# Kernel tuning notes

Hardware: AMD Instinct MI355X
Metric: run time of the kernel (lower is better)

## Reference

```python
import jax, jax.numpy as jnp
import numpy as np

B, S, D, H = 2, 2048, 1024, 16
DK = D // H


def setup_inputs() -> dict:
    key = jax.random.key(0)
    ks = jax.random.split(key, 11)
    scale = 1.0 / np.sqrt(D)
    inp = {
        "k": jax.random.normal(ks[0], (B, S, D), jnp.float32),
        "q": jax.random.normal(ks[1], (B, S, D), jnp.float32),
        "v": jax.random.normal(ks[2], (B, S, D), jnp.float32),
        "w_q": jax.random.normal(ks[3], (D, D), jnp.float32) * scale,
        "b_q": jax.random.normal(ks[4], (D,), jnp.float32) * 0.01,
        "w_k": jax.random.normal(ks[5], (D, D), jnp.float32) * scale,
        "b_k": jax.random.normal(ks[6], (D,), jnp.float32) * 0.01,
        "w_v": jax.random.normal(ks[7], (D, D), jnp.float32) * scale,
        "b_v": jax.random.normal(ks[8], (D,), jnp.float32) * 0.01,
        "w_o": jax.random.normal(ks[9], (D, D), jnp.float32) * scale,
        "b_o": jax.random.normal(ks[10], (D,), jnp.float32) * 0.01,
        # causal mask; positions with mask==0 get -1e9 (masked_fill semantics)
        "mask": jnp.tril(jnp.ones((1, 1, S, S), jnp.int32)),
    }
    return inp


def reference(k, q, v, w_q, b_q, w_k, b_k, w_v, b_v, w_o, b_o, mask):
    MINUS_INF = -1000000000.0

    def proj(x, w, b):
        # nn.Linear: x @ w.T + b, then split heads -> [B, H, S, DK]
        y = x @ w.T + b
        return y.reshape(B, S, H, DK).transpose(0, 2, 1, 3)

    Q = proj(q, w_q, b_q)
    K = proj(k, w_k, b_k)
    V = proj(v, w_v, b_v)

    # [B, H, Sq, Sk] scores
    scores = jnp.einsum("bhqd,bhkd->bhqk", Q, K) / jnp.sqrt(jnp.float32(DK))
    scores = jnp.where(mask == 0, MINUS_INF, scores)
    attn = jax.nn.softmax(scores, axis=-1)

    out = jnp.einsum("bhqk,bhkd->bhqd", attn, V)  # [B, H, S, DK]
    out = out.transpose(0, 2, 1, 3).reshape(B, S, D)  # concat heads
    return out @ w_o.T + b_o
```

## Files before the change

### kernel.cpp

```cpp
#include <hip/hip_runtime.h>

typedef __bf16 bf16;
typedef __bf16 v8bf __attribute__((ext_vector_type(8)));
typedef __bf16 v4bf __attribute__((ext_vector_type(4)));
typedef float  v4f  __attribute__((ext_vector_type(4)));

#define MFMA16(a,b,c) __builtin_amdgcn_mfma_f32_16x16x32_bf16((a),(b),(c),0,0,0)

static constexpr int Sq = 2048;
static constexpr size_t NI = 4194304;
static constexpr size_t NW = 1048576;

__device__ __forceinline__ void gld_lds16(const void* g, void* l) {
  __builtin_amdgcn_global_load_lds(
      (__attribute__((address_space(1))) unsigned int*)g,
      (__attribute__((address_space(3))) unsigned int*)l,
      16, 0, 0);
}

__global__ __launch_bounds__(256) void convert_kernel(
    const float* __restrict__ q, const float* __restrict__ k, const float* __restrict__ v,
    const float* __restrict__ wq, const float* __restrict__ wk,
    const float* __restrict__ wv, const float* __restrict__ wo,
    bf16* __restrict__ dst)
{
  const int NI4 = 1048576;
  const int NW4 = 262144;
  int idx = blockIdx.x * 256 + threadIdx.x;
  const float* src; size_t dstoff; int local;
  if (idx < 3 * NI4) {
    int a = idx >> 20; local = idx & (NI4 - 1);
    src = (a == 0) ? q : ((a == 1) ? k : v);
    dstoff = (size_t)a * NI;
  } else {
    int t = idx - 3 * NI4;
    int a = t >> 18; local = t & (NW4 - 1);
    src = (a == 0) ? wq : ((a == 1) ? wk : ((a == 2) ? wv : wo));
    dstoff = 3 * NI + (size_t)a * NW;
  }
  float4 f = ((const float4*)src)[local];
  v4bf hv = { (bf16)f.x, (bf16)f.y, (bf16)f.z, (bf16)f.w };
  *(v4bf*)(dst + dstoff + (size_t)local * 4) = hv;
}

__device__ __forceinline__ void gemm_bt_body(
    const bf16* __restrict__ A, const bf16* __restrict__ Bw,
    const float* __restrict__ bias, bf16* __restrict__ outh,
    float* __restrict__ outf, int bm, int bn, int mode)
{
  __shared__ alignas(16) bf16 As[128 * 32];
  __shared__ alignas(16) bf16 Bs[128 * 32];
  const int tid = threadIdx.x;
  const int wave = tid >> 6, lane = tid & 63;
  const int quad = lane >> 4, l15 = lane & 15;
  const int wm = (wave >> 1) * 64, wn = (wave & 1) * 64;
  const int lrow = lane >> 2, lcol = (lane & 3) * 8;

  v4f acc[4][4];
#pragma unroll
  for (int i = 0; i < 4; i++)
#pragma unroll
    for (int j = 0; j < 4; j++) { v4f z = {0.f, 0.f, 0.f, 0.f}; acc[i][j] = z; }

  const bf16* gA = A  + (size_t)(bm + wave * 32 + lrow) * 1024 + lcol;
  const bf16* gB = Bw + (size_t)(bn + wave * 32 + lrow) * 1024 + lcol;
  bf16* lA0 = &As[(wave * 32) * 32];
  bf16* lA1 = &As[(wave * 32 + 16) * 32];
  bf16* lB0 = &Bs[(wave * 32) * 32];
  bf16* lB1 = &Bs[(wave * 32 + 16) * 32];

  for (int k0 = 0; k0 < 1024; k0 += 32) {
    gld_lds16(gA + k0, lA0);
    gld_lds16(gA + 16 * 1024 + k0, lA1);
    gld_lds16(gB + k0, lB0);
    gld_lds16(gB + 16 * 1024 + k0, lB1);
    __syncthreads();
    v8bf af[4], bfr[4];
#pragma unroll
    for (int i = 0; i < 4; i++)
      af[i] = *(const v8bf*)&As[(wm + i * 16 + l15) * 32 + quad * 8];
#pragma unroll
    for (int j = 0; j < 4; j++)
      bfr[j] = *(const v8bf*)&Bs[(wn + j * 16 + l15) * 32 + quad * 8];
#pragma unroll
    for (int i = 0; i < 4; i++)
#pragma unroll
      for (int j = 0; j < 4; j++)
        acc[i][j] = MFMA16(af[i], bfr[j], acc[i][j]);
    __syncthreads();
  }

#pragma unroll
  for (int i = 0; i < 4; i++) {
    const int m0 = bm + wm + i * 16 + quad * 4;
#pragma unroll
    for (int j = 0; j < 4; j++) {
      const int n = bn + wn + j * 16 + l15;
      const float bv = bias[n];
      if (mode == 1) {
#pragma unroll
        for (int r = 0; r < 4; r++)
          outf[(size_t)(m0 + r) * 1024 + n] = acc[i][j][r] + bv;
      } else if (mode == 2) {
        int b_ = m0 >> 11, s_ = m0 & 2047;
        int h_ = n >> 6,  dk = n & 63;
        v4bf pk;
#pragma unroll
        for (int r = 0; r < 4; r++) pk[r] = (bf16)(acc[i][j][r] + bv);
        *(v4bf*)&outh[((size_t)((b_ * 16 + h_) * 64 + dk)) * 2048 + s_] = pk;
      } else {
        const float sc = (mode == 3) ? 0.18033688011112042f : 1.0f;
        int h_ = n >> 6,  dk = n & 63;
#pragma unroll
        for (int r = 0; r < 4; r++) {
          int m = m0 + r;
          int b_ = m >> 11, s_ = m & 2047;
          outh[(((size_t)(b_ * 16 + h_) * 2048 + s_) << 6) + dk] =
              (bf16)((acc[i][j][r] + bv) * sc);
        }
      }
    }
  }
}

__global__ __launch_bounds__(256, 2) void gemm_proj_kernel(
    const bf16* qb, const bf16* kb, const bf16* vb,
    const bf16* wqb, const bf16* wkb, const bf16* wvb,
    const float* bq, const float* bk, const float* bv,
    bf16* Qh, bf16* Kh, bf16* VhT)
{
  const bf16* A; const bf16* W; const float* bias; bf16* out; int mode;
  if (blockIdx.z == 0)      { A = qb; W = wqb; bias = bq; out = Qh;  mode = 3; }
  else if (blockIdx.z == 1) { A = kb; W = wkb; bias = bk; out = Kh;  mode = 0; }
  else                      { A = vb; W = wvb; bias = bv; out = VhT; mode = 2; }
  gemm_bt_body(A, W, bias, out, nullptr, blockIdx.y * 128, blockIdx.x * 128, mode);
}

__global__ __launch_bounds__(256, 2) void gemm_final_kernel(
    const bf16* Ob, const bf16* wob, const float* bo, float* out)
{
  gemm_bt_body(Ob, wob, bo, nullptr, out, blockIdx.y * 128, blockIdx.x * 128, 1);
}

__global__ __launch_bounds__(128, 2) void attn_kernel(
    const bf16* __restrict__ Qh, const bf16* __restrict__ Kh,
    const bf16* __restrict__ VhT, bf16* __restrict__ Ob)
{
  __shared__ alignas(16) bf16 Ps[2][16 * 72];
  const int tid = threadIdx.x;
  const int wave = tid >> 6, lane = tid & 63;
  const int quad = lane >> 4, l15 = lane & 15;
  const int bh = blockIdx.x, gy = blockIdx.y;
  const int b = bh >> 4, h = bh & 15;
  const int r8 = gy & 7, q8 = gy >> 3;
  const int u = 8 * q8 + ((q8 & 1) ? (7 - r8) : r8);
  const int qt = 2 * u + wave;
  const int L = u;
  const bf16* Qb = Qh + (size_t)bh * Sq * 64;
  const bf16* Kb = Kh + (size_t)bh * Sq * 64;
  const bf16* Vb = VhT + (size_t)bh * 64 * Sq;
  bf16* Pw = &Ps[wave][0];
  const int r0 = qt * 32;
  const int xk = l15 & 7;

  v8bf bq[2][2];
#pragma unroll
  for (int nt = 0; nt < 2; nt++)
#pragma unroll
    for (int ks = 0; ks < 2; ks++)
      bq[nt][ks] = *(const v8bf*)&Qb[(size_t)(r0 + nt * 16 + l15) * 64 + ks * 32 + quad * 8];

  float lsum[2] = {0.f, 0.f};
  v4f o[2][4];
#pragma unroll
  for (int nt = 0; nt < 2; nt++)
#pragma unroll
    for (int j = 0; j < 4; j++) { v4f z = {0.f, 0.f, 0.f, 0.f}; o[nt][j] = z; }

  auto loadK = [&](int kb, v8bf (&AK)[4][2]) {
#pragma unroll
    for (int m = 0; m < 4; m++) {
      AK[m][0] = *(const v8bf*)&Kb[(size_t)(kb + m * 16 + l15) * 64 + quad * 8];
      AK[m][1] = *(const v8bf*)&Kb[(size_t)(kb + m * 16 + l15) * 64 + 32 + quad * 8];
    }
  };
  auto loadV = [&](int kb, v8bf (&AV)[4][2]) {
#pragma unroll
    for (int j = 0; j < 4; j++) {
      AV[j][0] = *(const v8bf*)&Vb[(size_t)(j * 16 + l15) * 2048 + kb + quad * 8];
      AV[j][1] = *(const v8bf*)&Vb[(size_t)(j * 16 + l15) * 2048 + kb + 32 + quad * 8];
    }
  };
  auto compute = [&](const v8bf (&AK)[4][2], const v8bf (&AV)[4][2], int kc) {
    const int kbase = kc * 64;
    const bool diag = (kc == L);
#pragma unroll
    for (int nt = 0; nt < 2; nt++) {
      v4f cn[4];
#pragma unroll
      for (int m = 0; m < 4; m++) {
        v4f z = {0.f, 0.f, 0.f, 0.f};
        cn[m] = MFMA16(AK[m][0], bq[nt][0], z);
        cn[m] = MFMA16(AK[m][1], bq[nt][1], cn[m]);
      }
      const int qrow = r0 + nt * 16 + l15;
      const int rb = l15;
#pragma unroll
      for (int m = 0; m < 4; m++) {
        const int keyb = kbase + m * 16 + quad * 4;
        v4bf pk;
#pragma unroll
        for (int r = 0; r < 4; r++) {
          float e = exp2f(cn[m][r]);
          if (diag && (keyb + r > qrow)) e = 0.f;
          lsum[nt] += e;
          pk[r] = (bf16)e;
        }
        const int ch = (2 * m + (quad >> 1)) ^ xk;
        *(v4bf*)&Pw[rb * 72 + ch * 8 + (quad & 1) * 4] = pk;
      }
#pragma unroll
      for (int ks = 0; ks < 2; ks++) {
        const int ch = (4 * ks + quad) ^ xk;
        v8bf bp = *(const v8bf*)&Pw[rb * 72 + ch * 8];
#pragma unroll
        for (int j = 0; j < 4; j++)
          o[nt][j] = MFMA16(AV[j][ks], bp, o[nt][j]);
      }
    }
  };

  v8bf ak0[4][2], ak1[4][2], avv[4][2];
  loadK(0, ak0);
  int kc = 0;
  while (true) {
    loadV(kc * 64, avv);
    if (kc < L) loadK((kc + 1) * 64, ak1);
    compute(ak0, avv, kc);
    if (++kc > L) break;
    loadV(kc * 64, avv);
    if (kc < L) loadK((kc + 1) * 64, ak0);
    compute(ak1, avv, kc);
    if (++kc > L) break;
  }

#pragma unroll
  for (int nt = 0; nt < 2; nt++) {
    lsum[nt] += __shfl_xor(lsum[nt], 16, 64);
    lsum[nt] += __shfl_xor(lsum[nt], 32, 64);
  }
#pragma unroll
  for (int nt = 0; nt < 2; nt++) {
    const float inv = 1.0f / lsum[nt];
    const int qrow = r0 + nt * 16 + l15;
    bf16* dst = Ob + ((size_t)(b * Sq + qrow)) * 1024 + h * 64 + quad * 4;
#pragma unroll
    for (int j = 0; j < 4; j++) {
      v4bf pk;
#pragma unroll
      for (int r = 0; r < 4; r++) pk[r] = (bf16)(o[nt][j][r] * inv);
      *(v4bf*)(dst + j * 16) = pk;
    }
  }
}

extern "C" void kernel_launch(void* const* d_in, const int* in_sizes, int n_in,
                              void* d_out, int out_size, void* d_ws, size_t ws_size,
                              hipStream_t stream) {
  (void)in_sizes; (void)n_in; (void)out_size; (void)ws_size;
  const float* kin = (const float*)d_in[0];
  const float* qin = (const float*)d_in[1];
  const float* vin = (const float*)d_in[2];
  const float* wq  = (const float*)d_in[3];
  const float* bq  = (const float*)d_in[4];
  const float* wk  = (const float*)d_in[5];
  const float* bk  = (const float*)d_in[6];
  const float* wv  = (const float*)d_in[7];
  const float* bv  = (const float*)d_in[8];
  const float* wo  = (const float*)d_in[9];
  const float* bo  = (const float*)d_in[10];

  bf16* ws = (bf16*)d_ws;
  bf16* qb  = ws;
  bf16* kb  = ws + NI;
  bf16* vb  = ws + 2 * NI;
  bf16* wqb = ws + 3 * NI;
  bf16* wkb = wqb + NW;
  bf16* wvb = wqb + 2 * NW;
  bf16* wob = wqb + 3 * NW;
  bf16* Qh  = ws + 3 * NI + 4 * NW;
  bf16* Kh  = Qh + NI;
  bf16* VhT = Qh + 2 * NI;
  bf16* Ob  = Qh + 3 * NI;

  convert_kernel<<<16384, 256, 0, stream>>>(qin, kin, vin, wq, wk, wv, wo, ws);
  gemm_proj_kernel<<<dim3(8, 32, 3), 256, 0, stream>>>(
      qb, kb, vb, wqb, wkb, wvb, bq, bk, bv, Qh, Kh, VhT);
  attn_kernel<<<dim3(32, 32), 128, 0, stream>>>(Qh, Kh, VhT, Ob);
  gemm_final_kernel<<<dim3(8, 32), 256, 0, stream>>>(Ob, wob, bo, (float*)d_out);
}
```

Measured before the change: 269.9 us.

## Shrink attention per-wave query tile to 16 rows and double the grid

Each wave now handles 16 query rows instead of 32, and the block count along the query axis doubles to 64, with four query tiles sharing each 64-key causal block index. This exposes more parallelism and cuts per-wave register use (launch bound minimum-occupancy hint dropped). The cost is that every K/V tile loaded from global memory is reused across only half as many query rows, doubling K/V load traffic per unit of work. The P staging buffer padding is also removed, relying on the XOR swizzle alone for bank spreading.

```diff
diff --git a/kernel.cpp b/kernel.cpp
--- a/kernel.cpp
+++ b/kernel.cpp
@@ -142,40 +142,37 @@
   gemm_bt_body(Ob, wob, bo, nullptr, out, blockIdx.y * 128, blockIdx.x * 128, 1);
 }
 
-__global__ __launch_bounds__(128, 2) void attn_kernel(
+__global__ __launch_bounds__(128) void attn_kernel(
     const bf16* __restrict__ Qh, const bf16* __restrict__ Kh,
     const bf16* __restrict__ VhT, bf16* __restrict__ Ob)
 {
-  __shared__ alignas(16) bf16 Ps[2][16 * 72];
+  __shared__ alignas(16) bf16 Ps[2][16 * 64];
   const int tid = threadIdx.x;
   const int wave = tid >> 6, lane = tid & 63;
   const int quad = lane >> 4, l15 = lane & 15;
   const int bh = blockIdx.x, gy = blockIdx.y;
   const int b = bh >> 4, h = bh & 15;
-  const int r8 = gy & 7, q8 = gy >> 3;
-  const int u = 8 * q8 + ((q8 & 1) ? (7 - r8) : r8);
-  const int qt = 2 * u + wave;
-  const int L = u;
+  const int u = gy >> 1, e = gy & 1;
+  const int q8 = u >> 3, r8 = u & 7;
+  const int a = 8 * q8 + ((q8 & 1) ? (7 - r8) : r8);
+  const int qt = 4 * a + 2 * e + wave;
+  const int L = a;
   const bf16* Qb = Qh + (size_t)bh * Sq * 64;
   const bf16* Kb = Kh + (size_t)bh * Sq * 64;
   const bf16* Vb = VhT + (size_t)bh * 64 * Sq;
   bf16* Pw = &Ps[wave][0];
-  const int r0 = qt * 32;
+  const int r0 = qt * 16;
   const int xk = l15 & 7;
 
-  v8bf bq[2][2];
-#pragma unroll
-  for (int nt = 0; nt < 2; nt++)
-#pragma unroll
-    for (int ks = 0; ks < 2; ks++)
-      bq[nt][ks] = *(const v8bf*)&Qb[(size_t)(r0 + nt * 16 + l15) * 64 + ks * 32 + quad * 8];
-
-  float lsum[2] = {0.f, 0.f};
-  v4f o[2][4];
-#pragma unroll
-  for (int nt = 0; nt < 2; nt++)
-#pragma unroll
-    for (int j = 0; j < 4; j++) { v4f z = {0.f, 0.f, 0.f, 0.f}; o[nt][j] = z; }
+  v8bf bq[2];
+#pragma unroll
+  for (int ks = 0; ks < 2; ks++)
+    bq[ks] = *(const v8bf*)&Qb[(size_t)(r0 + l15) * 64 + ks * 32 + quad * 8];
+
+  float lsum = 0.f;
+  v4f o[4];
+#pragma unroll
+  for (int j = 0; j < 4; j++) { v4f z = {0.f, 0.f, 0.f, 0.f}; o[j] = z; }
 
   auto loadK = [&](int kb, v8bf (&AK)[4][2]) {
 #pragma unroll
@@ -194,39 +191,35 @@
   auto compute = [&](const v8bf (&AK)[4][2], const v8bf (&AV)[4][2], int kc) {
     const int kbase = kc * 64;
     const bool diag = (kc == L);
-#pragma unroll
-    for (int nt = 0; nt < 2; nt++) {
-      v4f cn[4];
-#pragma unroll
-      for (int m = 0; m < 4; m++) {
-        v4f z = {0.f, 0.f, 0.f, 0.f};
-        cn[m] = MFMA16(AK[m][0], bq[nt][0], z);
-        cn[m] = MFMA16(AK[m][1], bq[nt][1], cn[m]);
+    v4f cn[4];
+#pragma unroll
+    for (int m = 0; m < 4; m++) {
+      v4f z = {0.f, 0.f, 0.f, 0.f};
+      cn[m] = MFMA16(AK[m][0], bq[0], z);
+      cn[m] = MFMA16(AK[m][1], bq[1], cn[m]);
+    }
+    const int qrow = r0 + l15;
+#pragma unroll
+    for (int m = 0; m < 4; m++) {
+      const int keyb = kbase + m * 16 + quad * 4;
+      v4bf pk;
+#pragma unroll
+      for (int r = 0; r < 4; r++) {
+        float ev = exp2f(cn[m][r]);
+        if (diag && (keyb + r > qrow)) ev = 0.f;
+        lsum += ev;
+        pk[r] = (bf16)ev;
       }
-      const int qrow = r0 + nt * 16 + l15;
-      const int rb = l15;
-#pragma unroll
-      for (int m = 0; m < 4; m++) {
-        const int keyb = kbase + m * 16 + quad * 4;
-        v4bf pk;
-#pragma unroll
-        for (int r = 0; r < 4; r++) {
-          float e = exp2f(cn[m][r]);
-          if (diag && (keyb + r > qrow)) e = 0.f;
-          lsum[nt] += e;
-          pk[r] = (bf16)e;
-        }
-        const int ch = (2 * m + (quad >> 1)) ^ xk;
-        *(v4bf*)&Pw[rb * 72 + ch * 8 + (quad & 1) * 4] = pk;
-      }
-#pragma unroll
-      for (int ks = 0; ks < 2; ks++) {
-        const int ch = (4 * ks + quad) ^ xk;
-        v8bf bp = *(const v8bf*)&Pw[rb * 72 + ch * 8];
-#pragma unroll
-        for (int j = 0; j < 4; j++)
-          o[nt][j] = MFMA16(AV[j][ks], bp, o[nt][j]);
-      }
+      const int ch = (2 * m + (quad >> 1)) ^ xk;
+      *(v4bf*)&Pw[l15 * 64 + ch * 8 + (quad & 1) * 4] = pk;
+    }
+#pragma unroll
+    for (int ks = 0; ks < 2; ks++) {
+      const int ch = (4 * ks + quad) ^ xk;
+      v8bf bp = *(const v8bf*)&Pw[l15 * 64 + ch * 8];
+#pragma unroll
+      for (int j = 0; j < 4; j++)
+        o[j] = MFMA16(AV[j][ks], bp, o[j]);
     }
   };
 
@@ -244,23 +237,17 @@
     if (++kc > L) break;
   }
 
-#pragma unroll
-  for (int nt = 0; nt < 2; nt++) {
-    lsum[nt] += __shfl_xor(lsum[nt], 16, 64);
-    lsum[nt] += __shfl_xor(lsum[nt], 32, 64);
-  }
-#pragma unroll
-  for (int nt = 0; nt < 2; nt++) {
-    const float inv = 1.0f / lsum[nt];
-    const int qrow = r0 + nt * 16 + l15;
-    bf16* dst = Ob + ((size_t)(b * Sq + qrow)) * 1024 + h * 64 + quad * 4;
-#pragma unroll
-    for (int j = 0; j < 4; j++) {
-      v4bf pk;
-#pragma unroll
-      for (int r = 0; r < 4; r++) pk[r] = (bf16)(o[nt][j][r] * inv);
-      *(v4bf*)(dst + j * 16) = pk;
-    }
+  lsum += __shfl_xor(lsum, 16, 64);
+  lsum += __shfl_xor(lsum, 32, 64);
+  const float inv = 1.0f / lsum;
+  const int qrow = r0 + l15;
+  bf16* dst = Ob + ((size_t)(b * Sq + qrow)) * 1024 + h * 64 + quad * 4;
+#pragma unroll
+  for (int j = 0; j < 4; j++) {
+    v4bf pk;
+#pragma unroll
+    for (int r = 0; r < 4; r++) pk[r] = (bf16)(o[j][r] * inv);
+    *(v4bf*)(dst + j * 16) = pk;
   }
 }
 
@@ -296,6 +283,6 @@
   convert_kernel<<<16384, 256, 0, stream>>>(qin, kin, vin, wq, wk, wv, wo, ws);
   gemm_proj_kernel<<<dim3(8, 32, 3), 256, 0, stream>>>(
       qb, kb, vb, wqb, wkb, wvb, bq, bk, bv, Qh, Kh, VhT);
-  attn_kernel<<<dim3(32, 32), 128, 0, stream>>>(Qh, Kh, VhT, Ob);
+  attn_kernel<<<dim3(32, 64), 128, 0, stream>>>(Qh, Kh, VhT, Ob);
   gemm_final_kernel<<<dim3(8, 32), 256, 0, stream>>>(Ob, wob, bo, (float*)d_out);
 }
```

Measured after the change: 319.1 us. +18.3%, slower.
